# Optimization experiments

Hardware: AMD Instinct MI355X
Metric: run time of the kernel (lower is better)

## Reference

```python
import jax, jax.numpy as jnp
import numpy as np

B, F, D = 1024, 16, 64
P = F * (F - 1) // 2  # 120 field pairs


def setup_inputs() -> dict:
    key = jax.random.key(0)
    k1, k2, k3 = jax.random.split(key, 3)
    x = jax.random.normal(k1, (B, F, D), dtype=jnp.float32)
    # torch Linear weight layout: [out_features, in_features] = [D, D*D], one per pair
    W = jax.random.normal(k2, (P, D, D * D), dtype=jnp.float32) * (1.0 / np.sqrt(D * D))
    b = jax.random.normal(k3, (P, D), dtype=jnp.float32) * 0.01
    return {"x": x, "W": W, "b": b}


def reference(x, W, b):
    # x: [B, F, D]; W: [P, D, D*D]; b: [P, D]
    Bs, Fs, Ds = x.shape
    Ps = W.shape[0]
    ii, jj = np.triu_indices(Fs, k=1)  # pair order matches nested (i, j>i) loop
    xi = x[:, ii, :]  # [B, P, D] -> left vector of outer product
    xj = x[:, jj, :]  # [B, P, D] -> right vector
    # Flattened outer tmp[b, a*D + c] = xi[b,p,a] * xj[b,p,c];
    # Linear: out = tmp @ W^T + b. Reshape W to [P, D_out, a, c] and fuse,
    # never materializing the [B, P, D*D] outer-product tensor.
    W3 = W.reshape(Ps, Ds, Ds, Ds)
    out = jnp.einsum('bpa,bpc,pkac->bpk', xi, xj, W3) + b[None, :, :]
    return out  # [B, P, D]
```

## Files before the change

kernel.cpp:

```cpp
#include <hip/hip_runtime.h>
#include <stdint.h>
#include <stddef.h>

constexpr int NB = 1024;
constexpr int NF = 16;
constexpr int ND = 64;
constexpr int NP = 120;
constexpr int KD = ND * ND;
constexpr int OUT_STRIDE = NP * ND;

constexpr int BM = 256;

using floatx4 = __attribute__((ext_vector_type(4))) float;
using half8   = __attribute__((ext_vector_type(8))) _Float16;
using half2v  = __attribute__((ext_vector_type(2))) _Float16;
using fp16x2  = __attribute__((ext_vector_type(2))) __fp16;
using uint4v  = __attribute__((ext_vector_type(4))) uint32_t;
using ushort4v = __attribute__((ext_vector_type(4))) uint16_t;

constexpr int BT_STRIDE = ND;
constexpr int BT_BUF    = ND * BT_STRIDE;

__device__ __forceinline__ half2v pkh2(float f0, float f1) {
    fp16x2 h = __builtin_amdgcn_cvt_pkrtz(f0, f1);
    return __builtin_bit_cast(half2v, h);
}
__device__ __forceinline__ uint32_t pk16(float f0, float f1) {
    fp16x2 h = __builtin_amdgcn_cvt_pkrtz(f0, f1);
    return __builtin_bit_cast(uint32_t, h);
}
__device__ __forceinline__ uint16_t f16bits(float f) {
    return __builtin_bit_cast(uint16_t, (_Float16)f);
}

__device__ __forceinline__ void lds_barrier() {
    asm volatile("s_waitcnt lgkmcnt(0)" ::: "memory");
    __builtin_amdgcn_s_barrier();
    asm volatile("" ::: "memory");
}

__global__ __launch_bounds__(512, 4)
void outer_kernel(const float* __restrict__ x, const float* __restrict__ W,
                  const float* __restrict__ bias, float* __restrict__ out)
{
    __shared__ uint16_t lds_xit[ND * BM];
    __shared__ uint16_t lds_bt[2 * BT_BUF];

    const int p  = blockIdx.x;
    const int b0 = blockIdx.y * BM;

    int icol = 0, rem = p;
    while (rem >= NF - 1 - icol) { rem -= NF - 1 - icol; ++icol; }
    const int jcol = icol + 1 + rem;

    const int t    = threadIdx.x;
    const int wave = t >> 6;
    const int lane = t & 63;
    const int r    = lane & 15;
    const int quad = lane >> 4;
    const int wm   = wave & 3;
    const int wn   = wave >> 2;

    {
        const int mrow  = t >> 1;
        const int chalf = (t & 1) * 32;
        const int wms = mrow >> 6, mss = (mrow >> 4) & 3, rs = mrow & 15;
        const int dbase = wms * 64 + rs * 4 + mss;
        const float* src = x + (size_t)(b0 + mrow) * (NF * ND) + icol * ND + chalf;
        #pragma unroll
        for (int c = 0; c < 32; c += 4) {
            floatx4 v = *(const floatx4*)(src + c);
            lds_xit[(chalf + c + 0) * BM + dbase] = f16bits(v.x);
            lds_xit[(chalf + c + 1) * BM + dbase] = f16bits(v.y);
            lds_xit[(chalf + c + 2) * BM + dbase] = f16bits(v.z);
            lds_xit[(chalf + c + 3) * BM + dbase] = f16bits(v.w);
        }
    }

    half2v xjh[4][8];
    #pragma unroll
    for (int ms = 0; ms < 4; ++ms) {
        const float* srow = x + (size_t)(b0 + wm*64 + ms*16 + r) * (NF * ND)
                              + jcol * ND + quad * 8;
        #pragma unroll
        for (int ks = 0; ks < 2; ++ks) {
            floatx4 v0 = *(const floatx4*)(srow + ks * 32);
            floatx4 v1 = *(const floatx4*)(srow + ks * 32 + 4);
            xjh[ms][ks*4 + 0] = pkh2(v0.x, v0.y);
            xjh[ms][ks*4 + 1] = pkh2(v0.z, v0.w);
            xjh[ms][ks*4 + 2] = pkh2(v1.x, v1.y);
            xjh[ms][ks*4 + 3] = pkh2(v1.z, v1.w);
        }
    }

    const int n_st = t >> 3;
    const int cg   = t & 7;
    const float* wsrc = W + ((size_t)p * ND + n_st) * KD + cg * 8;
    uint16_t* bdst0 = &lds_bt[n_st * BT_STRIDE + ((cg ^ (n_st & 7)) * 8)];

    floatx4 wregA[2], wregB[2];

    wregA[0] = *(const floatx4*)(wsrc);
    wregA[1] = *(const floatx4*)(wsrc + 4);
    {
        uint4v q0 = (uint4v){ pk16(wregA[0].x, wregA[0].y), pk16(wregA[0].z, wregA[0].w),
                              pk16(wregA[1].x, wregA[1].y), pk16(wregA[1].z, wregA[1].w) };
        *(uint4v*)(bdst0) = q0;
    }
    wregA[0] = *(const floatx4*)(wsrc + ND);
    wregA[1] = *(const floatx4*)(wsrc + ND + 4);
    __syncthreads();

    floatx4 acc[4][2] = {};

    const int xg0 = (quad ^ (r & 7)) * 8;

    auto substep = [&](int a, int cur, floatx4* wC, floatx4* wN) {
        if (a + 1 < ND) {
            uint16_t* bd = bdst0 + (cur ^ 1) * BT_BUF;
            uint4v q0 = (uint4v){ pk16(wC[0].x, wC[0].y), pk16(wC[0].z, wC[0].w),
                                  pk16(wC[1].x, wC[1].y), pk16(wC[1].z, wC[1].w) };
            *(uint4v*)(bd) = q0;
        }
        if (a + 2 < ND) {
            const float* wn2 = wsrc + (size_t)(a + 2) * ND;
            wN[0] = *(const floatx4*)(wn2);
            wN[1] = *(const floatx4*)(wn2 + 4);
        }
        const uint16_t* rbuf = lds_bt + cur * BT_BUF;

        union { ushort4v s4; uint32_t u[2]; } xiu;
        xiu.s4 = *(const ushort4v*)&lds_xit[a * BM + wm * 64 + r * 4];

        half8 bfr[2][2];
        #pragma unroll
        for (int ns = 0; ns < 2; ++ns) {
            const int rowb = (wn*32 + ns*16 + r) * BT_STRIDE;
            bfr[ns][0] = *(const half8*)&rbuf[rowb + xg0];
            bfr[ns][1] = *(const half8*)&rbuf[rowb + (xg0 ^ 32)];
        }

        __builtin_amdgcn_s_setprio(1);
        #pragma unroll
        for (int ms = 0; ms < 4; ++ms) {
            const uint32_t xw = xiu.u[ms >> 1];
            const uint32_t sel = (ms & 1) ? 0x03020302u : 0x01000100u;
            half2v xs = __builtin_bit_cast(half2v, __builtin_amdgcn_perm(xw, xw, sel));
            union { half8 h8; half2v h2[4]; } u0, u1;
            #pragma unroll
            for (int q2 = 0; q2 < 4; ++q2) {
                u0.h2[q2] = xs * xjh[ms][q2];
                u1.h2[q2] = xs * xjh[ms][4 + q2];
            }
            #pragma unroll
            for (int ns = 0; ns < 2; ++ns) {
                acc[ms][ns] = __builtin_amdgcn_mfma_f32_16x16x32_f16(
                    u0.h8, bfr[ns][0], acc[ms][ns], 0, 0, 0);
                acc[ms][ns] = __builtin_amdgcn_mfma_f32_16x16x32_f16(
                    u1.h8, bfr[ns][1], acc[ms][ns], 0, 0, 0);
            }
        }
        __builtin_amdgcn_s_setprio(0);

        lds_barrier();
    };

    #pragma unroll 1
    for (int a = 0; a < ND; a += 2) {
        substep(a,     0, wregA, wregB);
        substep(a + 1, 1, wregB, wregA);
    }

    #pragma unroll
    for (int ns = 0; ns < 2; ++ns) {
        const float bb = bias[p * ND + wn*32 + ns*16 + r];
        #pragma unroll
        for (int ms = 0; ms < 4; ++ms) {
            #pragma unroll
            for (int reg = 0; reg < 4; ++reg) {
                const int row = b0 + wm*64 + ms*16 + quad*4 + reg;
                out[(size_t)row * OUT_STRIDE + p * ND + wn*32 + ns*16 + r]
                    = acc[ms][ns][reg] + bb;
            }
        }
    }
}

extern "C" void kernel_launch(void* const* d_in, const int* in_sizes, int n_in,
                              void* d_out, int out_size, void* d_ws, size_t ws_size,
                              hipStream_t stream) {
    const float* x    = (const float*)d_in[0];
    const float* W    = (const float*)d_in[1];
    const float* bias = (const float*)d_in[2];
    float* out = (float*)d_out;

    dim3 grid(NP, NB / BM);
    outer_kernel<<<grid, 512, 0, stream>>>(x, W, bias, out);
}
```

Before: 217.8 us.

## Prefetch LDS fragments one step ahead with quad-buffered weight tiles

```diff
diff --git a/kernel.cpp b/kernel.cpp
--- a/kernel.cpp
+++ b/kernel.cpp
@@ -20,6 +20,7 @@
 
 constexpr int BT_STRIDE = ND;
 constexpr int BT_BUF    = ND * BT_STRIDE;
+constexpr int NBUF      = 4;
 
 __device__ __forceinline__ half2v pkh2(float f0, float f1) {
     fp16x2 h = __builtin_amdgcn_cvt_pkrtz(f0, f1);
@@ -38,13 +39,15 @@
     __builtin_amdgcn_s_barrier();
     asm volatile("" ::: "memory");
 }
+
+struct XiU { uint32_t u[2]; };
 
 __global__ __launch_bounds__(512, 4)
 void outer_kernel(const float* __restrict__ x, const float* __restrict__ W,
                   const float* __restrict__ bias, float* __restrict__ out)
 {
     __shared__ uint16_t lds_xit[ND * BM];
-    __shared__ uint16_t lds_bt[2 * BT_BUF];
+    __shared__ uint16_t lds_bt[NBUF * BT_BUF];
 
     const int p  = blockIdx.x;
     const int b0 = blockIdx.y * BM;
@@ -98,52 +101,39 @@
     const float* wsrc = W + ((size_t)p * ND + n_st) * KD + cg * 8;
     uint16_t* bdst0 = &lds_bt[n_st * BT_STRIDE + ((cg ^ (n_st & 7)) * 8)];
 
-    floatx4 wregA[2], wregB[2];
-
-    wregA[0] = *(const floatx4*)(wsrc);
-    wregA[1] = *(const floatx4*)(wsrc + 4);
-    {
-        uint4v q0 = (uint4v){ pk16(wregA[0].x, wregA[0].y), pk16(wregA[0].z, wregA[0].w),
-                              pk16(wregA[1].x, wregA[1].y), pk16(wregA[1].z, wregA[1].w) };
-        *(uint4v*)(bdst0) = q0;
-    }
-    wregA[0] = *(const floatx4*)(wsrc + ND);
-    wregA[1] = *(const floatx4*)(wsrc + ND + 4);
-    __syncthreads();
-
-    floatx4 acc[4][2] = {};
-
     const int xg0 = (quad ^ (r & 7)) * 8;
 
-    auto substep = [&](int a, int cur, floatx4* wC, floatx4* wN) {
-        if (a + 1 < ND) {
-            uint16_t* bd = bdst0 + (cur ^ 1) * BT_BUF;
-            uint4v q0 = (uint4v){ pk16(wC[0].x, wC[0].y), pk16(wC[0].z, wC[0].w),
-                                  pk16(wC[1].x, wC[1].y), pk16(wC[1].z, wC[1].w) };
-            *(uint4v*)(bd) = q0;
-        }
-        if (a + 2 < ND) {
-            const float* wn2 = wsrc + (size_t)(a + 2) * ND;
-            wN[0] = *(const floatx4*)(wn2);
-            wN[1] = *(const floatx4*)(wn2 + 4);
-        }
-        const uint16_t* rbuf = lds_bt + cur * BT_BUF;
-
-        union { ushort4v s4; uint32_t u[2]; } xiu;
-        xiu.s4 = *(const ushort4v*)&lds_xit[a * BM + wm * 64 + r * 4];
-
-        half8 bfr[2][2];
+    auto packW = [&](int a2, const floatx4* wC) {
+        uint16_t* bd = bdst0 + (a2 & 3) * BT_BUF;
+        uint4v q0 = (uint4v){ pk16(wC[0].x, wC[0].y), pk16(wC[0].z, wC[0].w),
+                              pk16(wC[1].x, wC[1].y), pk16(wC[1].z, wC[1].w) };
+        *(uint4v*)(bd) = q0;
+    };
+    auto loadW = [&](int a3, floatx4* wD) {
+        const float* wp = wsrc + (size_t)a3 * ND;
+        wD[0] = *(const floatx4*)(wp);
+        wD[1] = *(const floatx4*)(wp + 4);
+    };
+    auto readfrags = [&](int a, half8 (&bfr)[2][2], XiU& xi) {
+        const uint16_t* rbuf = lds_bt + (a & 3) * BT_BUF;
+        union { ushort4v s4; uint32_t u[2]; } xu;
+        xu.s4 = *(const ushort4v*)&lds_xit[a * BM + wm * 64 + r * 4];
+        xi.u[0] = xu.u[0]; xi.u[1] = xu.u[1];
         #pragma unroll
         for (int ns = 0; ns < 2; ++ns) {
             const int rowb = (wn*32 + ns*16 + r) * BT_STRIDE;
             bfr[ns][0] = *(const half8*)&rbuf[rowb + xg0];
             bfr[ns][1] = *(const half8*)&rbuf[rowb + (xg0 ^ 32)];
         }
-
+    };
+
+    floatx4 acc[4][2] = {};
+
+    auto compute = [&](const half8 (&bfr)[2][2], const XiU& xi) {
         __builtin_amdgcn_s_setprio(1);
         #pragma unroll
         for (int ms = 0; ms < 4; ++ms) {
-            const uint32_t xw = xiu.u[ms >> 1];
+            const uint32_t xw = xi.u[ms >> 1];
             const uint32_t sel = (ms & 1) ? 0x03020302u : 0x01000100u;
             half2v xs = __builtin_bit_cast(half2v, __builtin_amdgcn_perm(xw, xw, sel));
             union { half8 h8; half2v h2[4]; } u0, u1;
@@ -161,14 +151,32 @@
             }
         }
         __builtin_amdgcn_s_setprio(0);
-
-        lds_barrier();
-    };
+    };
+
+    floatx4 wreg[2], wtmp[2];
+    loadW(0, wreg);
+    loadW(1, wtmp);
+    packW(0, wreg);
+    packW(1, wtmp);
+    loadW(2, wreg);
+    lds_barrier();
+
+    half8 bfrA[2][2], bfrB[2][2];
+    XiU xiA, xiB;
+    readfrags(0, bfrA, xiA);
 
     #pragma unroll 1
     for (int a = 0; a < ND; a += 2) {
-        substep(a,     0, wregA, wregB);
-        substep(a + 1, 1, wregB, wregA);
+        if (a + 2 < ND) packW(a + 2, wreg);
+        if (a + 3 < ND) loadW(a + 3, wreg);
+        if (a + 1 < ND) readfrags(a + 1, bfrB, xiB);
+        compute(bfrA, xiA);
+        lds_barrier();
+        if (a + 3 < ND) packW(a + 3, wreg);
+        if (a + 4 < ND) loadW(a + 4, wreg);
+        if (a + 2 < ND) readfrags(a + 2, bfrA, xiA);
+        compute(bfrB, xiB);
+        lds_barrier();
     }
 
     #pragma unroll
```

Result: slower. 222.5 us (+2.1%).

## Switch to 32x32x16 MFMA tiles and stage two W columns per barrier

Applied to the files above, without the earlier changes.

```diff
diff --git a/kernel.cpp b/kernel.cpp
--- a/kernel.cpp
+++ b/kernel.cpp
@@ -10,16 +10,17 @@
 constexpr int OUT_STRIDE = NP * ND;
 
 constexpr int BM = 256;
+constexpr int NS = 32;
 
-using floatx4 = __attribute__((ext_vector_type(4))) float;
-using half8   = __attribute__((ext_vector_type(8))) _Float16;
-using half2v  = __attribute__((ext_vector_type(2))) _Float16;
-using fp16x2  = __attribute__((ext_vector_type(2))) __fp16;
-using uint4v  = __attribute__((ext_vector_type(4))) uint32_t;
-using ushort4v = __attribute__((ext_vector_type(4))) uint16_t;
+using floatx4  = __attribute__((ext_vector_type(4))) float;
+using floatx16 = __attribute__((ext_vector_type(16))) float;
+using half8    = __attribute__((ext_vector_type(8))) _Float16;
+using half2v   = __attribute__((ext_vector_type(2))) _Float16;
+using fp16x2   = __attribute__((ext_vector_type(2))) __fp16;
+using uint4v   = __attribute__((ext_vector_type(4))) uint32_t;
 
-constexpr int BT_STRIDE = ND;
-constexpr int BT_BUF    = ND * BT_STRIDE;
+constexpr int WCOL = ND * ND / 64 * 64;
+constexpr int WSTG = 2 * WCOL;
 
 __device__ __forceinline__ half2v pkh2(float f0, float f1) {
     fp16x2 h = __builtin_amdgcn_cvt_pkrtz(f0, f1);
@@ -44,7 +45,7 @@
                   const float* __restrict__ bias, float* __restrict__ out)
 {
     __shared__ uint16_t lds_xit[ND * BM];
-    __shared__ uint16_t lds_bt[2 * BT_BUF];
+    __shared__ uint16_t lds_bt[2 * WSTG];
 
     const int p  = blockIdx.x;
     const int b0 = blockIdx.y * BM;
@@ -56,16 +57,15 @@
     const int t    = threadIdx.x;
     const int wave = t >> 6;
     const int lane = t & 63;
-    const int r    = lane & 15;
-    const int quad = lane >> 4;
+    const int r32  = lane & 31;
+    const int kh   = lane >> 5;
     const int wm   = wave & 3;
     const int wn   = wave >> 2;
 
     {
         const int mrow  = t >> 1;
         const int chalf = (t & 1) * 32;
-        const int wms = mrow >> 6, mss = (mrow >> 4) & 3, rs = mrow & 15;
-        const int dbase = wms * 64 + rs * 4 + mss;
+        const int dbase = (mrow >> 6) * 64 + (mrow & 31) * 2 + ((mrow >> 5) & 1);
         const float* src = x + (size_t)(b0 + mrow) * (NF * ND) + icol * ND + chalf;
         #pragma unroll
         for (int c = 0; c < 32; c += 4) {
@@ -77,111 +77,108 @@
         }
     }
 
-    half2v xjh[4][8];
+    half2v xjh[2][16];
     #pragma unroll
-    for (int ms = 0; ms < 4; ++ms) {
-        const float* srow = x + (size_t)(b0 + wm*64 + ms*16 + r) * (NF * ND)
-                              + jcol * ND + quad * 8;
+    for (int mt = 0; mt < 2; ++mt) {
+        const float* srow = x + (size_t)(b0 + wm*64 + mt*32 + r32) * (NF * ND)
+                              + jcol * ND + kh * 8;
         #pragma unroll
-        for (int ks = 0; ks < 2; ++ks) {
-            floatx4 v0 = *(const floatx4*)(srow + ks * 32);
-            floatx4 v1 = *(const floatx4*)(srow + ks * 32 + 4);
-            xjh[ms][ks*4 + 0] = pkh2(v0.x, v0.y);
-            xjh[ms][ks*4 + 1] = pkh2(v0.z, v0.w);
-            xjh[ms][ks*4 + 2] = pkh2(v1.x, v1.y);
-            xjh[ms][ks*4 + 3] = pkh2(v1.z, v1.w);
+        for (int kc = 0; kc < 4; ++kc) {
+            floatx4 v0 = *(const floatx4*)(srow + kc * 16);
+            floatx4 v1 = *(const floatx4*)(srow + kc * 16 + 4);
+            xjh[mt][kc*4 + 0] = pkh2(v0.x, v0.y);
+            xjh[mt][kc*4 + 1] = pkh2(v0.z, v0.w);
+            xjh[mt][kc*4 + 2] = pkh2(v1.x, v1.y);
+            xjh[mt][kc*4 + 3] = pkh2(v1.z, v1.w);
         }
     }
 
     const int n_st = t >> 3;
     const int cg   = t & 7;
     const float* wsrc = W + ((size_t)p * ND + n_st) * KD + cg * 8;
-    uint16_t* bdst0 = &lds_bt[n_st * BT_STRIDE + ((cg ^ (n_st & 7)) * 8)];
+    uint16_t* bdst0 = &lds_bt[n_st * ND + ((cg ^ (n_st & 7)) * 8)];
 
-    floatx4 wregA[2], wregB[2];
-
-    wregA[0] = *(const floatx4*)(wsrc);
-    wregA[1] = *(const floatx4*)(wsrc + 4);
-    {
-        uint4v q0 = (uint4v){ pk16(wregA[0].x, wregA[0].y), pk16(wregA[0].z, wregA[0].w),
-                              pk16(wregA[1].x, wregA[1].y), pk16(wregA[1].z, wregA[1].w) };
-        *(uint4v*)(bdst0) = q0;
-    }
-    wregA[0] = *(const floatx4*)(wsrc + ND);
-    wregA[1] = *(const floatx4*)(wsrc + ND + 4);
-    __syncthreads();
-
-    floatx4 acc[4][2] = {};
-
-    const int xg0 = (quad ^ (r & 7)) * 8;
-
-    auto substep = [&](int a, int cur, floatx4* wC, floatx4* wN) {
-        if (a + 1 < ND) {
-            uint16_t* bd = bdst0 + (cur ^ 1) * BT_BUF;
-            uint4v q0 = (uint4v){ pk16(wC[0].x, wC[0].y), pk16(wC[0].z, wC[0].w),
-                                  pk16(wC[1].x, wC[1].y), pk16(wC[1].z, wC[1].w) };
+    auto loadW2 = [&](int s2, floatx4* w) {
+        const float* wp = wsrc + (size_t)(2 * s2) * ND;
+        w[0] = *(const floatx4*)(wp);
+        w[1] = *(const floatx4*)(wp + 4);
+        w[2] = *(const floatx4*)(wp + ND);
+        w[3] = *(const floatx4*)(wp + ND + 4);
+    };
+    auto packW2 = [&](int d, const floatx4* w) {
+        #pragma unroll
+        for (int sub = 0; sub < 2; ++sub) {
+            uint16_t* bd = bdst0 + d * WSTG + sub * WCOL;
+            uint4v q0 = (uint4v){ pk16(w[sub*2].x,   w[sub*2].y),   pk16(w[sub*2].z,   w[sub*2].w),
+                                  pk16(w[sub*2+1].x, w[sub*2+1].y), pk16(w[sub*2+1].z, w[sub*2+1].w) };
             *(uint4v*)(bd) = q0;
         }
-        if (a + 2 < ND) {
-            const float* wn2 = wsrc + (size_t)(a + 2) * ND;
-            wN[0] = *(const floatx4*)(wn2);
-            wN[1] = *(const floatx4*)(wn2 + 4);
-        }
-        const uint16_t* rbuf = lds_bt + cur * BT_BUF;
+    };
 
-        union { ushort4v s4; uint32_t u[2]; } xiu;
-        xiu.s4 = *(const ushort4v*)&lds_xit[a * BM + wm * 64 + r * 4];
+    floatx16 acc[2] = {};
 
-        half8 bfr[2][2];
-        #pragma unroll
-        for (int ns = 0; ns < 2; ++ns) {
-            const int rowb = (wn*32 + ns*16 + r) * BT_STRIDE;
-            bfr[ns][0] = *(const half8*)&rbuf[rowb + xg0];
-            bfr[ns][1] = *(const half8*)&rbuf[rowb + (xg0 ^ 32)];
-        }
+    const int nrow   = wn*32 + r32;
+    const int bbase  = nrow * ND;
+    const int bswz   = (r32 & 7);
+
+    auto compute = [&](int s, int cur) {
+        const int a0 = 2 * s;
+        const uint16_t* rb = lds_bt + cur * WSTG;
+
+        const uint32_t xi0 = *(const uint32_t*)&lds_xit[a0 * BM + wm*64 + r32*2];
+        const uint32_t xi1 = *(const uint32_t*)&lds_xit[(a0 + 1) * BM + wm*64 + r32*2];
+        const half2v xs00 = __builtin_bit_cast(half2v, __builtin_amdgcn_perm(xi0, xi0, 0x01000100u));
+        const half2v xs01 = __builtin_bit_cast(half2v, __builtin_amdgcn_perm(xi0, xi0, 0x03020302u));
+        const half2v xs10 = __builtin_bit_cast(half2v, __builtin_amdgcn_perm(xi1, xi1, 0x01000100u));
+        const half2v xs11 = __builtin_bit_cast(half2v, __builtin_amdgcn_perm(xi1, xi1, 0x03020302u));
 
         __builtin_amdgcn_s_setprio(1);
         #pragma unroll
-        for (int ms = 0; ms < 4; ++ms) {
-            const uint32_t xw = xiu.u[ms >> 1];
-            const uint32_t sel = (ms & 1) ? 0x03020302u : 0x01000100u;
-            half2v xs = __builtin_bit_cast(half2v, __builtin_amdgcn_perm(xw, xw, sel));
-            union { half8 h8; half2v h2[4]; } u0, u1;
+        for (int kc = 0; kc < 4; ++kc) {
+            const int boff = bbase + (((2*kc + kh) ^ bswz) * 8);
+            half8 bf0 = *(const half8*)&rb[boff];
+            half8 bf1 = *(const half8*)&rb[WCOL + boff];
+
+            union { half8 h8; half2v h2[4]; } a00, a01, a10, a11;
             #pragma unroll
-            for (int q2 = 0; q2 < 4; ++q2) {
-                u0.h2[q2] = xs * xjh[ms][q2];
-                u1.h2[q2] = xs * xjh[ms][4 + q2];
+            for (int q = 0; q < 4; ++q) {
+                const half2v xv = xjh[0][kc*4 + q];
+                const half2v yv = xjh[1][kc*4 + q];
+                a00.h2[q] = xs00 * xv;
+                a10.h2[q] = xs10 * xv;
+                a01.h2[q] = xs01 * yv;
+                a11.h2[q] = xs11 * yv;
             }
-            #pragma unroll
-            for (int ns = 0; ns < 2; ++ns) {
-                acc[ms][ns] = __builtin_amdgcn_mfma_f32_16x16x32_f16(
-                    u0.h8, bfr[ns][0], acc[ms][ns], 0, 0, 0);
-                acc[ms][ns] = __builtin_amdgcn_mfma_f32_16x16x32_f16(
-                    u1.h8, bfr[ns][1], acc[ms][ns], 0, 0, 0);
-            }
+            acc[0] = __builtin_amdgcn_mfma_f32_32x32x16_f16(a00.h8, bf0, acc[0], 0, 0, 0);
+            acc[1] = __builtin_amdgcn_mfma_f32_32x32x16_f16(a01.h8, bf0, acc[1], 0, 0, 0);
+            acc[0] = __builtin_amdgcn_mfma_f32_32x32x16_f16(a10.h8, bf1, acc[0], 0, 0, 0);
+            acc[1] = __builtin_amdgcn_mfma_f32_32x32x16_f16(a11.h8, bf1, acc[1], 0, 0, 0);
         }
         __builtin_amdgcn_s_setprio(0);
-
-        lds_barrier();
     };
 
+    floatx4 wpk[4], wtmp[4];
+    loadW2(0, wtmp);
+    packW2(0, wtmp);
+    loadW2(1, wpk);
+    __syncthreads();
+
     #pragma unroll 1
-    for (int a = 0; a < ND; a += 2) {
-        substep(a,     0, wregA, wregB);
-        substep(a + 1, 1, wregB, wregA);
+    for (int s = 0; s < NS; ++s) {
+        const int cur = s & 1;
+        if (s + 1 < NS) packW2(cur ^ 1, wpk);
+        if (s + 2 < NS) loadW2(s + 2, wpk);
+        compute(s, cur);
+        lds_barrier();
     }
 
+    const float bb = bias[p * ND + wn*32 + r32];
     #pragma unroll
-    for (int ns = 0; ns < 2; ++ns) {
-        const float bb = bias[p * ND + wn*32 + ns*16 + r];
+    for (int mt = 0; mt < 2; ++mt) {
         #pragma unroll
-        for (int ms = 0; ms < 4; ++ms) {
-            #pragma unroll
-            for (int reg = 0; reg < 4; ++reg) {
-                const int row = b0 + wm*64 + ms*16 + quad*4 + reg;
-                out[(size_t)row * OUT_STRIDE + p * ND + wn*32 + ns*16 + r]
-                    = acc[ms][ns][reg] + bb;
-            }
+        for (int reg = 0; reg < 16; ++reg) {
+            const int row = b0 + wm*64 + mt*32 + (reg & 3) + 8*(reg >> 2) + 4*kh;
+            out[(size_t)row * OUT_STRIDE + p * ND + wn*32 + r32] = acc[mt][reg] + bb;
         }
     }
 }
```

Measured after the change: 225.9 us. +3.7%, slower.
